# Optimization experiments

Hardware: AMD Instinct MI355X
Metric: run time of the kernel (lower is better)

## Reference

```python
import jax, jax.numpy as jnp
import numpy as np

N = 4096  # square [B, T+1] as required by original indexing (T = shape[0], indexed on dim 1)
GAMMA = 0.99

def setup_inputs() -> dict:
    key = jax.random.key(0)
    ks = jax.random.split(key, 6)
    shape = (N, N)
    names = ["Q", "expected_target_Q", "target_Q", "rewards",
             "target_policy_probs", "behaviour_policy_probs"]
    return {n: jax.random.normal(k, shape, dtype=jnp.float32) for n, k in zip(names, ks)}

def _retrace_loss(Q, expected_target_Q, target_Q, rewards,
                  target_policy_probs, behaviour_policy_probs):
    rewards = rewards * 100.0
    # retrace weights c_t = exp(min(log pi - log b, 0)) = min(1, pi/b)
    c_ret = jnp.exp(jnp.minimum(target_policy_probs - behaviour_policy_probs, 0.0))
    T = Q.shape[0]  # faithful to original (square inputs => equals time length)
    last = target_Q[:, T - 1]  # Q_ret[:, -1] = target_Q[:, -1]
    # reverse-time linear recurrence via a single scan:
    # Q_ret[t-1] = r[t-1] + gamma*c[t]*(Q_ret[t] - target_Q[t]) + gamma*E[t]
    xs = (rewards[:, :T - 1].T[::-1],          # [T-1, B], t-1 = T-2 .. 0
          c_ret[:, 1:T].T[::-1],               # c[t],  t = T-1 .. 1
          target_Q[:, 1:T].T[::-1],
          expected_target_Q[:, 1:T].T[::-1])

    def step(q_next, x):
        r, c, tq, eq = x
        q = r + GAMMA * c * (q_next - tq) + GAMMA * eq
        return q, q

    _, qs = jax.lax.scan(step, last, xs)       # qs: [T-1, B] for t = T-2 .. 0
    Q_ret = jnp.concatenate([qs[::-1].T, last[:, None]], axis=1)  # [B, T]
    Q_ret = jax.lax.stop_gradient(Q_ret)       # computed under torch.no_grad()
    return jnp.mean((Q - Q_ret) ** 2)

def reference(Q, expected_target_Q, target_Q, rewards,
              target_policy_probs, behaviour_policy_probs):
    return _retrace_loss(Q, expected_target_Q, target_Q, rewards,
                         target_policy_probs, behaviour_policy_probs)
```

## Files before the change

### kernel.cpp

```cpp
#include <hip/hip_runtime.h>


#define NROWS 4096
#define TLEN  4096
#define BLOCK 1024
#define EPT   4
#define NWV   (BLOCK / 64)

__global__ __launch_bounds__(BLOCK) void retrace_main(
    const float* __restrict__ Q,
    const float* __restrict__ eQ,
    const float* __restrict__ tQ,
    const float* __restrict__ rw,
    const float* __restrict__ tpp,
    const float* __restrict__ bpp,
    double* __restrict__ partials)
{
    constexpr float G = 0.99f;
    __shared__ float sWA[NWV], sWB[NWV];
    __shared__ float sRed[NWV];

    const int tid  = threadIdx.x;
    const int lane = tid & 63;
    const int wv   = tid >> 6;
    const long long base = (long long)blockIdx.x * TLEN;
    const int ua = EPT * tid;

    float4 Tv4, Pv4, Qt4, Ev4, Rv4, Qm4;
    Tv4 = *(const float4*)(tpp + base + ua);
    Pv4 = *(const float4*)(bpp + base + ua);
    Qt4 = *(const float4*)(tQ  + base + ua);
    Ev4 = *(const float4*)(eQ  + base + ua);
    Rv4 = *(const float4*)(rw  + base + ua);

    const bool bnd = (lane == 63) && (tid != BLOCK - 1);
    float bt = 0.f, bp = 0.f, bq = 0.f, be = 0.f;
    if (bnd) {
        bt = tpp[base + ua + EPT];
        bp = bpp[base + ua + EPT];
        bq = tQ [base + ua + EPT];
        be = eQ [base + ua + EPT];
    }

    Qm4 = *(const float4*)(Q + base + ua);

    __builtin_amdgcn_sched_barrier(0);

    float tv[4] = {Tv4.x, Tv4.y, Tv4.z, Tv4.w};
    float pv[4] = {Pv4.x, Pv4.y, Pv4.z, Pv4.w};
    float qv[4] = {Qt4.x, Qt4.y, Qt4.z, Qt4.w};
    float ev[4] = {Ev4.x, Ev4.y, Ev4.z, Ev4.w};
    float rv[4] = {Rv4.x, Rv4.y, Rv4.z, Rv4.w};
    float qm[4] = {Qm4.x, Qm4.y, Qm4.z, Qm4.w};

    float Aa[4], Bb[4];
    #pragma unroll
    for (int k = 0; k < 3; ++k) {
        const float c  = __expf(fminf(tv[k+1] - pv[k+1], 0.0f));
        const float gc = G * c;
        const float f  = fmaf(-gc, qv[k+1], G * ev[k+1]);
        Aa[k] = gc;
        Bb[k] = fmaf(100.0f, rv[k], f);
    }
    {
        float t4 = __shfl_down(tv[0], 1, 64);
        float p4 = __shfl_down(pv[0], 1, 64);
        float q4 = __shfl_down(qv[0], 1, 64);
        float e4 = __shfl_down(ev[0], 1, 64);
        if (bnd) { t4 = bt; p4 = bp; q4 = bq; e4 = be; }
        if (tid == BLOCK - 1) {
            Aa[3] = 0.0f;
            Bb[3] = qv[3];
        } else {
            const float c  = __expf(fminf(t4 - p4, 0.0f));
            const float gc = G * c;
            const float f  = fmaf(-gc, q4, G * e4);
            Aa[3] = gc;
            Bb[3] = fmaf(100.0f, rv[3], f);
        }
    }

    float Ac = 1.0f, Bc = 0.0f;
    #pragma unroll
    for (int k = 3; k >= 0; --k) {
        Bc = fmaf(Aa[k], Bc, Bb[k]);
        Ac = Aa[k] * Ac;
    }

    float Ai = Ac, Bi = Bc;
    #pragma unroll
    for (int off = 1; off < 64; off <<= 1) {
        const float Ap = __shfl_down(Ai, off, 64);
        const float Bp = __shfl_down(Bi, off, 64);
        if (lane < 64 - off) {
            Bi = fmaf(Ai, Bp, Bi);
            Ai = Ai * Ap;
        }
    }

    if (lane == 0) { sWA[wv] = Ai; sWB[wv] = Bi; }
    __syncthreads();
    float Bp = 0.0f;
    #pragma unroll
    for (int j = NWV - 1; j >= 1; --j)
        if (j > wv) Bp = fmaf(sWA[j], Bp, sWB[j]);

    float Ae = __shfl_down(Ai, 1, 64);
    float Be = __shfl_down(Bi, 1, 64);
    if (lane == 63) { Ae = 1.0f; Be = 0.0f; }
    float y = fmaf(Ae, Bp, Be);

    float acc = 0.0f;
    #pragma unroll
    for (int k = 3; k >= 0; --k) {
        y = fmaf(Aa[k], y, Bb[k]);
        const float d = qm[k] - y;
        acc = fmaf(d, d, acc);
    }

    #pragma unroll
    for (int off = 32; off > 0; off >>= 1)
        acc += __shfl_down(acc, off, 64);
    if (lane == 0) sRed[wv] = acc;
    __syncthreads();
    if (tid == 0) {
        float s = 0.0f;
        #pragma unroll
        for (int j = 0; j < NWV; ++j) s += sRed[j];
        partials[blockIdx.x] = (double)s;
    }
}

#define FBLOCK 1024

__global__ __launch_bounds__(FBLOCK) void retrace_finalize(
    const double* __restrict__ partials, float* __restrict__ out)
{
    __shared__ double sRed[FBLOCK / 64];
    double s = 0.0;
    #pragma unroll
    for (int i = 0; i < NROWS / FBLOCK; ++i)
        s += partials[threadIdx.x + i * FBLOCK];
    #pragma unroll
    for (int off = 32; off > 0; off >>= 1)
        s += __shfl_down(s, off, 64);
    if ((threadIdx.x & 63) == 0) sRed[threadIdx.x >> 6] = s;
    __syncthreads();
    if (threadIdx.x == 0) {
        double tot = 0.0;
        #pragma unroll
        for (int j = 0; j < FBLOCK / 64; ++j) tot += sRed[j];
        out[0] = (float)(tot / ((double)NROWS * (double)TLEN));
    }
}

extern "C" void kernel_launch(void* const* d_in, const int* in_sizes, int n_in,
                              void* d_out, int out_size, void* d_ws, size_t ws_size,
                              hipStream_t stream)
{
    const float* Q   = (const float*)d_in[0];
    const float* eQ  = (const float*)d_in[1];
    const float* tQ  = (const float*)d_in[2];
    const float* rw  = (const float*)d_in[3];
    const float* tpp = (const float*)d_in[4];
    const float* bpp = (const float*)d_in[5];
    double* partials = (double*)d_ws;

    retrace_main<<<NROWS, BLOCK, 0, stream>>>(Q, eQ, tQ, rw, tpp, bpp, partials);
    retrace_finalize<<<1, FBLOCK, 0, stream>>>(partials, (float*)d_out);
}
```

Before: 338.2 us.

## Make retrace kernel persistent with double-buffered row prefetch

Launches 256 blocks instead of one per row. Each block loops over 16 rows and issues the global loads for the next row into a second register buffer while it computes the current row's scan and loss. The aim is to hide memory latency behind the per-row shuffle and barrier chain, and to cut block launch overhead. In exchange, each thread holds roughly twice as many live registers, and each CU gets fewer resident blocks, since the grid now has one 1024-thread block per CU.

After: 338.6 us. About the same (+0.1%).

```diff
diff --git a/kernel.cpp b/kernel.cpp
--- a/kernel.cpp
+++ b/kernel.cpp
@@ -6,52 +6,48 @@
 #define BLOCK 1024
 #define EPT   4
 #define NWV   (BLOCK / 64)
-
-__global__ __launch_bounds__(BLOCK) void retrace_main(
-    const float* __restrict__ Q,
-    const float* __restrict__ eQ,
-    const float* __restrict__ tQ,
-    const float* __restrict__ rw,
-    const float* __restrict__ tpp,
-    const float* __restrict__ bpp,
-    double* __restrict__ partials)
+#define GRID  256
+#define RPB   (NROWS / GRID)
+
+struct RowBuf {
+    float4 T, P, Qt, E, Rw, Qm;
+    float bt, bp, bq, be;
+};
+
+__device__ __forceinline__ void issue_row(
+    RowBuf& b,
+    const float* __restrict__ Q,  const float* __restrict__ eQ,
+    const float* __restrict__ tQ, const float* __restrict__ rw,
+    const float* __restrict__ tpp, const float* __restrict__ bpp,
+    long long base, int ua, bool bnd)
+{
+    b.T  = *(const float4*)(tpp + base + ua);
+    b.P  = *(const float4*)(bpp + base + ua);
+    b.Qt = *(const float4*)(tQ  + base + ua);
+    b.E  = *(const float4*)(eQ  + base + ua);
+    b.Rw = *(const float4*)(rw  + base + ua);
+    b.Qm = *(const float4*)(Q   + base + ua);
+    if (bnd) {
+        b.bt = tpp[base + ua + EPT];
+        b.bp = bpp[base + ua + EPT];
+        b.bq = tQ [base + ua + EPT];
+        b.be = eQ [base + ua + EPT];
+    }
+}
+
+__device__ __forceinline__ void compute_row(
+    const RowBuf& b, int row, double* __restrict__ partials,
+    float* sWA, float* sWB, float* sRed,
+    int tid, int lane, int wv, bool bnd)
 {
     constexpr float G = 0.99f;
-    __shared__ float sWA[NWV], sWB[NWV];
-    __shared__ float sRed[NWV];
-
-    const int tid  = threadIdx.x;
-    const int lane = tid & 63;
-    const int wv   = tid >> 6;
-    const long long base = (long long)blockIdx.x * TLEN;
-    const int ua = EPT * tid;
-
-    float4 Tv4, Pv4, Qt4, Ev4, Rv4, Qm4;
-    Tv4 = *(const float4*)(tpp + base + ua);
-    Pv4 = *(const float4*)(bpp + base + ua);
-    Qt4 = *(const float4*)(tQ  + base + ua);
-    Ev4 = *(const float4*)(eQ  + base + ua);
-    Rv4 = *(const float4*)(rw  + base + ua);
-
-    const bool bnd = (lane == 63) && (tid != BLOCK - 1);
-    float bt = 0.f, bp = 0.f, bq = 0.f, be = 0.f;
-    if (bnd) {
-        bt = tpp[base + ua + EPT];
-        bp = bpp[base + ua + EPT];
-        bq = tQ [base + ua + EPT];
-        be = eQ [base + ua + EPT];
-    }
-
-    Qm4 = *(const float4*)(Q + base + ua);
-
-    __builtin_amdgcn_sched_barrier(0);
-
-    float tv[4] = {Tv4.x, Tv4.y, Tv4.z, Tv4.w};
-    float pv[4] = {Pv4.x, Pv4.y, Pv4.z, Pv4.w};
-    float qv[4] = {Qt4.x, Qt4.y, Qt4.z, Qt4.w};
-    float ev[4] = {Ev4.x, Ev4.y, Ev4.z, Ev4.w};
-    float rv[4] = {Rv4.x, Rv4.y, Rv4.z, Rv4.w};
-    float qm[4] = {Qm4.x, Qm4.y, Qm4.z, Qm4.w};
+
+    const float tv[4] = {b.T.x,  b.T.y,  b.T.z,  b.T.w};
+    const float pv[4] = {b.P.x,  b.P.y,  b.P.z,  b.P.w};
+    const float qv[4] = {b.Qt.x, b.Qt.y, b.Qt.z, b.Qt.w};
+    const float ev[4] = {b.E.x,  b.E.y,  b.E.z,  b.E.w};
+    const float rv[4] = {b.Rw.x, b.Rw.y, b.Rw.z, b.Rw.w};
+    const float qm[4] = {b.Qm.x, b.Qm.y, b.Qm.z, b.Qm.w};
 
     float Aa[4], Bb[4];
     #pragma unroll
@@ -67,7 +63,7 @@
         float p4 = __shfl_down(pv[0], 1, 64);
         float q4 = __shfl_down(qv[0], 1, 64);
         float e4 = __shfl_down(ev[0], 1, 64);
-        if (bnd) { t4 = bt; p4 = bp; q4 = bq; e4 = be; }
+        if (bnd) { t4 = b.bt; p4 = b.bp; q4 = b.bq; e4 = b.be; }
         if (tid == BLOCK - 1) {
             Aa[3] = 0.0f;
             Bb[3] = qv[3];
@@ -127,7 +123,43 @@
         float s = 0.0f;
         #pragma unroll
         for (int j = 0; j < NWV; ++j) s += sRed[j];
-        partials[blockIdx.x] = (double)s;
+        partials[row] = (double)s;
+    }
+}
+
+__global__ __launch_bounds__(BLOCK) void retrace_main(
+    const float* __restrict__ Q,
+    const float* __restrict__ eQ,
+    const float* __restrict__ tQ,
+    const float* __restrict__ rw,
+    const float* __restrict__ tpp,
+    const float* __restrict__ bpp,
+    double* __restrict__ partials)
+{
+    __shared__ float sWA[NWV], sWB[NWV], sRed[NWV];
+
+    const int tid  = threadIdx.x;
+    const int lane = tid & 63;
+    const int wv   = tid >> 6;
+    const int ua   = EPT * tid;
+    const bool bnd = (lane == 63) && (tid != BLOCK - 1);
+
+    RowBuf bufA, bufB;
+
+    issue_row(bufA, Q, eQ, tQ, rw, tpp, bpp,
+              (long long)blockIdx.x * TLEN, ua, bnd);
+
+    #pragma unroll
+    for (int j = 0; j < RPB; ++j) {
+        const int row = blockIdx.x + j * GRID;
+        if (j + 1 < RPB) {
+            const long long basen = (long long)(blockIdx.x + (j + 1) * GRID) * TLEN;
+            if ((j & 1) == 0) issue_row(bufB, Q, eQ, tQ, rw, tpp, bpp, basen, ua, bnd);
+            else              issue_row(bufA, Q, eQ, tQ, rw, tpp, bpp, basen, ua, bnd);
+        }
+        __builtin_amdgcn_sched_barrier(0);
+        if ((j & 1) == 0) compute_row(bufA, row, partials, sWA, sWB, sRed, tid, lane, wv, bnd);
+        else              compute_row(bufB, row, partials, sWA, sWB, sRed, tid, lane, wv, bnd);
     }
 }
 
@@ -166,6 +198,6 @@
     const float* bpp = (const float*)d_in[5];
     double* partials = (double*)d_ws;
 
-    retrace_main<<<NROWS, BLOCK, 0, stream>>>(Q, eQ, tQ, rw, tpp, bpp, partials);
+    retrace_main<<<GRID, BLOCK, 0, stream>>>(Q, eQ, tQ, rw, tpp, bpp, partials);
     retrace_finalize<<<1, FBLOCK, 0, stream>>>(partials, (float*)d_out);
 }
```
